# Kernel optimization log

Hardware: AMD Instinct MI355X
Metric: run time of the kernel (lower is better)

Reference implementation:

```python
import jax, jax.numpy as jnp
import numpy as np

BS, NQ, D, NH, NP, L, DFF = 4, 1024, 256, 8, 4, 6, 1024
H_BEV, W_BEV = 200, 150
NV = H_BEV * W_BEV
DH = D // NH


def setup_inputs() -> dict:
    key = jax.random.key(0)
    ks = iter(jax.random.split(key, 64))
    r = lambda *s: jax.random.normal(next(ks), s, dtype=jnp.float32)
    return {
        'query': r(BS, NQ, D),
        'query_pos': r(BS, NQ, D),
        'reference_points': jax.random.uniform(next(ks), (BS, NQ, 1, 2), dtype=jnp.float32),
        'src': r(BS, NV, D),
        'spatial_shapes': jnp.array([[H_BEV, W_BEV]], dtype=jnp.int32),
        'level_start_index': jnp.array([0], dtype=jnp.int32),
        'sa_in_w': r(L, 3 * D, D) * 0.02, 'sa_in_b': jnp.zeros((L, 3 * D), jnp.float32),
        'sa_out_w': r(L, D, D) * 0.02, 'sa_out_b': jnp.zeros((L, D), jnp.float32),
        'ca_off_w': r(L, NH * NP * 2, D) * 0.01, 'ca_off_b': r(L, NH * NP * 2) * 0.5,
        'ca_aw_w': r(L, NH * NP, D) * 0.01, 'ca_aw_b': jnp.zeros((L, NH * NP), jnp.float32),
        'ca_val_w': r(L, D, D) * 0.02, 'ca_val_b': jnp.zeros((L, D), jnp.float32),
        'ca_out_w': r(L, D, D) * 0.02, 'ca_out_b': jnp.zeros((L, D), jnp.float32),
        'n1_w': jnp.ones((L, D), jnp.float32), 'n1_b': jnp.zeros((L, D), jnp.float32),
        'n2_w': jnp.ones((L, D), jnp.float32), 'n2_b': jnp.zeros((L, D), jnp.float32),
        'n3_w': jnp.ones((L, D), jnp.float32), 'n3_b': jnp.zeros((L, D), jnp.float32),
        'ff1_w': r(L, DFF, D) * 0.02, 'ff1_b': jnp.zeros((L, DFF), jnp.float32),
        'ff2_w': r(L, D, DFF) * 0.02, 'ff2_b': jnp.zeros((L, D), jnp.float32),
    }


def layer_norm(x, w, b, eps=1e-5):
    m = jnp.mean(x, -1, keepdims=True)
    v = jnp.mean(jnp.square(x - m), -1, keepdims=True)
    return (x - m) / jnp.sqrt(v + eps) * w + b


def mha_self(x_qk, x_v, in_w, in_b, out_w, out_b):
    bs, nq, d = x_qk.shape
    qw, kw, vw = jnp.split(in_w, 3, axis=0)
    qb, kb, vb = jnp.split(in_b, 3, axis=0)
    q = (x_qk @ qw.T + qb).reshape(bs, nq, NH, DH)
    k = (x_qk @ kw.T + kb).reshape(bs, nq, NH, DH)
    v = (x_v @ vw.T + vb).reshape(bs, nq, NH, DH)
    att = jax.nn.softmax(jnp.einsum('bqhd,bkhd->bhqk', q, k) / jnp.sqrt(jnp.float32(DH)), axis=-1)
    o = jnp.einsum('bhqk,bkhd->bqhd', att, v).reshape(bs, nq, d)
    return o @ out_w.T + out_b


def msda(q, ref, src, lsi0, off_w, off_b, aw_w, aw_b, val_w, val_b, out_w, out_b):
    # single-level (n_levels=1) multi-scale deformable attention, grid_sample
    # bilinear with align_corners=False and zero padding, as in mmcv.
    bs, nq, d = q.shape
    v = (src @ val_w.T + val_b).reshape(bs, NV, NH, DH)
    vt = v.transpose(0, 2, 1, 3)  # (bs, NH, NV, DH)
    off = (q @ off_w.T + off_b).reshape(bs, nq, NH, NP, 2)
    aw = jax.nn.softmax((q @ aw_w.T + aw_b).reshape(bs, nq, NH, NP), axis=-1)
    norm = jnp.array([W_BEV, H_BEV], dtype=q.dtype)  # offset_normalizer = (W, H)
    loc = ref[:, :, None, 0, None, :] + off / norm  # (bs, nq, NH, NP, 2) in [0,1]
    x = loc[..., 0] * W_BEV - 0.5
    y = loc[..., 1] * H_BEV - 0.5
    x0 = jnp.floor(x)
    y0 = jnp.floor(y)
    acc = jnp.zeros((bs, NH, nq, NP, DH), q.dtype)
    for dx, dy in ((0, 0), (1, 0), (0, 1), (1, 1)):
        xi = x0 + dx
        yi = y0 + dy
        w = (1.0 - jnp.abs(x - xi)) * (1.0 - jnp.abs(y - yi))
        valid = (xi >= 0) & (xi < W_BEV) & (yi >= 0) & (yi < H_BEV)
        w = jnp.where(valid, w, 0.0)  # (bs, nq, NH, NP)
        xi_c = jnp.clip(xi, 0, W_BEV - 1).astype(jnp.int32)
        yi_c = jnp.clip(yi, 0, H_BEV - 1).astype(jnp.int32)
        idx = lsi0 + yi_c * W_BEV + xi_c  # flat index into NV
        idx_t = idx.transpose(0, 2, 1, 3).reshape(bs, NH, nq * NP)
        g = jnp.take_along_axis(vt, idx_t[..., None], axis=2).reshape(bs, NH, nq, NP, DH)
        acc = acc + g * w.transpose(0, 2, 1, 3)[..., None]
    o = jnp.einsum('bhqpd,bqhp->bqhd', acc, aw).reshape(bs, nq, d)
    return o @ out_w.T + out_b


def _forward(query, query_pos, reference_points, src,
             sa_in_w, sa_in_b, sa_out_w, sa_out_b,
             ca_off_w, ca_off_b, ca_aw_w, ca_aw_b, ca_val_w, ca_val_b, ca_out_w, ca_out_b,
             n1_w, n1_b, n2_w, n2_b, n3_w, n3_b,
             ff1_w, ff1_b, ff2_w, ff2_b,
             spatial_shapes, level_start_index):
    lsi0 = level_start_index[0]
    out = query
    inter = []
    for l in range(L):
        qk = out + query_pos
        sa = mha_self(qk, out, sa_in_w[l], sa_in_b[l], sa_out_w[l], sa_out_b[l])
        out = layer_norm(out + sa, n2_w[l], n2_b[l])
        ca = msda(out + query_pos, reference_points, src, lsi0,
                  ca_off_w[l], ca_off_b[l], ca_aw_w[l], ca_aw_b[l],
                  ca_val_w[l], ca_val_b[l], ca_out_w[l], ca_out_b[l])
        out = layer_norm(out + ca, n1_w[l], n1_b[l])
        ff = jax.nn.relu(out @ ff1_w[l].T + ff1_b[l]) @ ff2_w[l].T + ff2_b[l]
        out = layer_norm(out + ff, n3_w[l], n3_b[l])
        inter.append(out)
    hs = jnp.stack(inter)  # (L, bs, nq, D)
    refs = jnp.stack([reference_points] * L)  # (L, bs, nq, 1, 2)
    return hs, refs


def reference(query, query_pos, reference_points, src, spatial_shapes, level_start_index,
              sa_in_w, sa_in_b, sa_out_w, sa_out_b,
              ca_off_w, ca_off_b, ca_aw_w, ca_aw_b, ca_val_w, ca_val_b, ca_out_w, ca_out_b,
              n1_w, n1_b, n2_w, n2_b, n3_w, n3_b,
              ff1_w, ff1_b, ff2_w, ff2_b):
    return _forward(query, query_pos, reference_points, src,
                    sa_in_w, sa_in_b, sa_out_w, sa_out_b,
                    ca_off_w, ca_off_b, ca_aw_w, ca_aw_b, ca_val_w, ca_val_b, ca_out_w, ca_out_b,
                    n1_w, n1_b, n2_w, n2_b, n3_w, n3_b,
                    ff1_w, ff1_b, ff2_w, ff2_b,
                    spatial_shapes, level_start_index)
```

## Files before the change

### kernel.cpp

```cpp
#include <hip/hip_runtime.h>

typedef __attribute__((ext_vector_type(8))) short short8;
typedef __attribute__((ext_vector_type(4))) float f32x4;
typedef unsigned short u16;

#define DEVI static __device__ __forceinline__

DEVI float b2f(u16 u){ unsigned int x = ((unsigned int)u) << 16; float f; __builtin_memcpy(&f, &x, 4); return f; }
DEVI u16 f2b(float f){ unsigned int u; __builtin_memcpy(&u, &f, 4); u += 0x7fffu + ((u >> 16) & 1u); return (u16)(u >> 16); }
DEVI short8 cvt8(const float* __restrict__ p){
  f32x4 a = *(const f32x4*)p;
  f32x4 b = *(const f32x4*)(p + 4);
  short8 r;
  r[0]=(short)f2b(a[0]); r[1]=(short)f2b(a[1]); r[2]=(short)f2b(a[2]); r[3]=(short)f2b(a[3]);
  r[4]=(short)f2b(b[0]); r[5]=(short)f2b(b[1]); r[6]=(short)f2b(b[2]); r[7]=(short)f2b(b[3]);
  return r;
}

__global__ __launch_bounds__(256) void cvtall_k(
    const float* __restrict__ sa_in_w, const float* __restrict__ sa_out_w,
    const float* __restrict__ val_w,   const float* __restrict__ cout_w,
    const float* __restrict__ ff1w,    const float* __restrict__ ff2w,
    const float* __restrict__ off_w,   const float* __restrict__ aw_w,
    const float* __restrict__ off_b,   const float* __restrict__ aw_b,
    const float* __restrict__ src,
    u16* __restrict__ wsa_b, u16* __restrict__ wsao_b, u16* __restrict__ wval_b,
    u16* __restrict__ wcao_b, u16* __restrict__ wff1_b, u16* __restrict__ wff2_b,
    u16* __restrict__ wofaw, float* __restrict__ obc, u16* __restrict__ src_b)
{
  long u = (long)blockIdx.x * 256 + threadIdx.x;
  if (u < 147456) { ((short8*)wsa_b)[u]  = cvt8(sa_in_w  + u * 8); return; } u -= 147456;
  if (u < 49152)  { ((short8*)wsao_b)[u] = cvt8(sa_out_w + u * 8); return; } u -= 49152;
  if (u < 49152)  { ((short8*)wval_b)[u] = cvt8(val_w    + u * 8); return; } u -= 49152;
  if (u < 49152)  { ((short8*)wcao_b)[u] = cvt8(cout_w   + u * 8); return; } u -= 49152;
  if (u < 196608) { ((short8*)wff1_b)[u] = cvt8(ff1w     + u * 8); return; } u -= 196608;
  if (u < 196608) { ((short8*)wff2_b)[u] = cvt8(ff2w     + u * 8); return; } u -= 196608;
  if (u < 12288)  { long e = u * 8; int l = (int)(e >> 14); long rem = e & 16383;
                    ((short8*)wofaw)[(l * 24576 + rem) >> 3] = cvt8(off_w + e); return; } u -= 12288;
  if (u < 6144)   { long e = u * 8; int l = (int)(e >> 13); long rem = e & 8191;
                    ((short8*)wofaw)[(l * 24576 + 16384 + rem) >> 3] = cvt8(aw_w + e); return; } u -= 6144;
  if (u < 3840000){ ((short8*)src_b)[u]  = cvt8(src + u * 8); return; } u -= 3840000;
  if (u < 72) {
    long e0 = u * 8;
#pragma unroll
    for (int j = 0; j < 8; j++) {
      long e = e0 + j;
      if (e < 384) { int l = (int)(e >> 6); obc[l * 96 + (e & 63)] = off_b[e]; }
      else { long e2 = e - 384; int l = (int)(e2 >> 5); obc[l * 96 + 64 + (e2 & 31)] = aw_b[e2]; }
    }
  }
}

template<int MT, bool RELU, bool OUTBF, bool VT, bool LN>
__global__ __launch_bounds__(256) void gemm_w_k(
    const u16* __restrict__ A, int lda,
    const u16* __restrict__ W, long wZ,
    const float* __restrict__ bias, int bZ,
    void* __restrict__ Cv, int ldo, long cZ,
    int K,
    u16* __restrict__ vt,
    const float* __restrict__ res,
    const float* __restrict__ lnw, const float* __restrict__ lnb,
    const float* __restrict__ qpos,
    float* __restrict__ out_f, u16* __restrict__ out_b16,
    u16* __restrict__ qk_b16, float* __restrict__ hsp)
{
  __shared__ u16 As[32 * MT * 8];
  __shared__ float r1s[4][64], r2s[4][64], mArr[64], iArr[64];
  const int wave = threadIdx.x >> 6, lane = threadIdx.x & 63;
  const int bm = blockIdx.x * MT;
  const int bn = blockIdx.y * 256 + wave * 64;
  const int lr = lane & 15, lq = lane >> 4;
  constexpr int SH = (MT == 64) ? 6 : 5;
  const u16* Wz = W + (long)blockIdx.z * wZ;
  const float* bz = bias + (long)blockIdx.z * bZ;
  f32x4 acc[MT / 16][4] = {};
  const int nchunks = K >> 8;
  for (int ch = 0; ch < nchunks; ch++) {
#pragma unroll
    for (int it = 0; it < MT / 8; it++) {
      int ub = wave * (MT * 8) + it * 64;
      int u = ub + lane;
      int row = u & (MT - 1), kgrp = u >> SH;
      const u16* ga = A + (long)(bm + row) * lda + ch * 256 + kgrp * 8;
      __builtin_amdgcn_global_load_lds(
          (const __attribute__((address_space(1))) void*)ga,
          (__attribute__((address_space(3))) void*)(As + ub * 8), 16, 0, 0);
    }
    __syncthreads();
#pragma unroll
    for (int s = 0; s < 8; s++) {
      short8 af[MT / 16], bf[4];
#pragma unroll
      for (int i = 0; i < MT / 16; i++)
        af[i] = *(const short8*)(As + ((s * 4 + lq) * MT + i * 16 + lr) * 8);
#pragma unroll
      for (int j = 0; j < 4; j++) {
        int cc = bn + j * 16 + lr;
        bf[j] = *(const short8*)(Wz + (long)cc * K + ch * 256 + s * 32 + lq * 8);
      }
#pragma unroll
      for (int i = 0; i < MT / 16; i++)
#pragma unroll
        for (int j = 0; j < 4; j++)
          acc[i][j] = __builtin_amdgcn_mfma_f32_16x16x32_bf16(af[i], bf[j], acc[i][j], 0, 0, 0);
    }
    __syncthreads();
  }

  float bv[4];
#pragma unroll
  for (int j = 0; j < 4; j++) bv[j] = bz[bn + j * 16 + lr];

  if (!LN) {
    char* Cz = (char*)Cv;
#pragma unroll
    for (int j = 0; j < 4; j++) {
      int cc = bn + j * 16 + lr;
#pragma unroll
      for (int i = 0; i < MT / 16; i++) {
#pragma unroll
        for (int r = 0; r < 4; r++) {
          int rr = bm + i * 16 + lq * 4 + r;
          float v = acc[i][j][r] + bv[j];
          if (RELU) v = fmaxf(v, 0.f);
          long idx = (long)blockIdx.z * cZ + (long)rr * ldo + cc;
          if (OUTBF) ((u16*)Cz)[idx] = f2b(v);
          else       ((float*)Cz)[idx] = v;
          if (VT) {
            int b_ = rr >> 10, q_ = rr & 1023, h_ = cc >> 5, dh_ = cc & 31;
            vt[(long)((((b_ << 3) + h_) << 5) + dh_) * 1024 + q_] = f2b(v);
          }
        }
      }
    }
  } else {
    float s1[MT / 16][4] = {}, s2[MT / 16][4] = {};
#pragma unroll
    for (int i = 0; i < MT / 16; i++) {
#pragma unroll
      for (int r = 0; r < 4; r++) {
        int rowg = bm + i * 16 + lq * 4 + r;
#pragma unroll
        for (int j = 0; j < 4; j++) {
          int cc = bn + j * 16 + lr;
          float x = acc[i][j][r] + bv[j] + res[(long)rowg * 256 + cc];
          s1[i][r] += x; s2[i][r] += x * x;
        }
      }
    }
#pragma unroll
    for (int i = 0; i < MT / 16; i++)
#pragma unroll
      for (int r = 0; r < 4; r++) {
#pragma unroll
        for (int m = 1; m <= 8; m <<= 1) {
          s1[i][r] += __shfl_xor(s1[i][r], m);
          s2[i][r] += __shfl_xor(s2[i][r], m);
        }
      }
    if (lr == 0) {
#pragma unroll
      for (int i = 0; i < MT / 16; i++)
#pragma unroll
        for (int r = 0; r < 4; r++) {
          int rl = i * 16 + lq * 4 + r;
          r1s[wave][rl] = s1[i][r];
          r2s[wave][rl] = s2[i][r];
        }
    }
    __syncthreads();
    if (threadIdx.x < MT) {
      int t = threadIdx.x;
      float a = r1s[0][t] + r1s[1][t] + r1s[2][t] + r1s[3][t];
      float b = r2s[0][t] + r2s[1][t] + r2s[2][t] + r2s[3][t];
      float m = a * (1.f / 256.f);
      float var = b * (1.f / 256.f) - m * m;
      mArr[t] = m;
      iArr[t] = rsqrtf(var + 1e-5f);
    }
    __syncthreads();
#pragma unroll
    for (int i = 0; i < MT / 16; i++) {
#pragma unroll
      for (int r = 0; r < 4; r++) {
        int rl = i * 16 + lq * 4 + r;
        int rowg = bm + rl;
        float m = mArr[rl], inv = iArr[rl];
#pragma unroll
        for (int j = 0; j < 4; j++) {
          int cc = bn + j * 16 + lr;
          long idx = (long)rowg * 256 + cc;
          float x = acc[i][j][r] + bv[j] + res[idx];
          float y = (x - m) * inv * lnw[cc] + lnb[cc];
          out_f[idx] = y;
          if (out_b16) out_b16[idx] = f2b(y);
          if (qk_b16)  qk_b16[idx]  = f2b(y + qpos[idx]);
          if (hsp)     hsp[idx]     = y;
        }
      }
    }
  }
}

__global__ __launch_bounds__(256) void qkv_k(
    const u16* __restrict__ qk_b, const u16* __restrict__ out_b,
    const u16* __restrict__ wsa, const float* __restrict__ bsa,
    u16* __restrict__ qkbuf, u16* __restrict__ vt)
{
  __shared__ u16 As[32 * 64 * 8];
  const int sel = blockIdx.y;
  const u16* A = (sel == 2) ? out_b : qk_b;
  const u16* W = wsa + (long)sel * 256 * 256;
  const int wave = threadIdx.x >> 6, lane = threadIdx.x & 63;
  const int bm = blockIdx.x * 64;
  const int bn = wave * 64;
  const int lr = lane & 15, lq = lane >> 4;
  f32x4 acc[4][4] = {};
#pragma unroll
  for (int it = 0; it < 8; it++) {
    int ub = wave * 512 + it * 64;
    int u = ub + lane;
    int row = u & 63, kgrp = u >> 6;
    const u16* ga = A + (long)(bm + row) * 256 + kgrp * 8;
    __builtin_amdgcn_global_load_lds(
        (const __attribute__((address_space(1))) void*)ga,
        (__attribute__((address_space(3))) void*)(As + ub * 8), 16, 0, 0);
  }
  __syncthreads();
#pragma unroll
  for (int s = 0; s < 8; s++) {
    short8 af[4], bf[4];
#pragma unroll
    for (int i = 0; i < 4; i++)
      af[i] = *(const short8*)(As + ((s * 4 + lq) * 64 + i * 16 + lr) * 8);
#pragma unroll
    for (int j = 0; j < 4; j++) {
      int cc = bn + j * 16 + lr;
      bf[j] = *(const short8*)(W + (long)cc * 256 + s * 32 + lq * 8);
    }
#pragma unroll
    for (int i = 0; i < 4; i++)
#pragma unroll
      for (int j = 0; j < 4; j++)
        acc[i][j] = __builtin_amdgcn_mfma_f32_16x16x32_bf16(af[i], bf[j], acc[i][j], 0, 0, 0);
  }
  float bv[4];
#pragma unroll
  for (int j = 0; j < 4; j++) bv[j] = bsa[sel * 256 + bn + j * 16 + lr];
#pragma unroll
  for (int j = 0; j < 4; j++) {
    int cc = bn + j * 16 + lr;
#pragma unroll
    for (int i = 0; i < 4; i++) {
#pragma unroll
      for (int r = 0; r < 4; r++) {
        int rr = bm + i * 16 + lq * 4 + r;
        float v = acc[i][j][r] + bv[j];
        if (sel < 2) {
          qkbuf[(long)rr * 512 + sel * 256 + cc] = f2b(v);
        } else {
          int b_ = rr >> 10, q_ = rr & 1023, h_ = cc >> 5, dh_ = cc & 31;
          vt[(long)((((b_ << 3) + h_) << 5) + dh_) * 1024 + q_] = f2b(v);
        }
      }
    }
  }
}

__global__ __launch_bounds__(256) void flash_k(
    const u16* __restrict__ qkbuf, const u16* __restrict__ vt,
    u16* __restrict__ obuf)
{
  const float SC = 0.17677669529663687f;
  __shared__ u16 Plds[4][32][136];
  const int bh = blockIdx.x >> 3;
  const int b = bh >> 3, h = bh & 7;
  const int qt = blockIdx.x & 7;
  const int wave = threadIdx.x >> 6, lane = threadIdx.x & 63;
  const int lr = lane & 15, lq = lane >> 4;
  const int qbase = qt * 128 + wave * 32;

  short8 qf[2];
#pragma unroll
  for (int i = 0; i < 2; i++)
    qf[i] = *(const short8*)(qkbuf + (long)(b * 1024 + qbase + i * 16 + lr) * 512 + h * 32 + lq * 8);

  const u16* Kb = qkbuf + (long)b * 1024 * 512 + 256 + h * 32;
  const u16* Vb = vt + (long)bh * 32 * 1024;

  f32x4 acc_o[2][2] = {};
  float m_run[2][4], l_run[2][4];
#pragma unroll
  for (int i = 0; i < 2; i++)
#pragma unroll
    for (int r = 0; r < 4; r++){ m_run[i][r] = -3e38f; l_run[i][r] = 0.f; }

  for (int kt = 0; kt < 8; kt++) {
    f32x4 s[2][8] = {};
#pragma unroll
    for (int j = 0; j < 8; j++) {
      short8 kf = *(const short8*)(Kb + (long)(kt * 128 + j * 16 + lr) * 512 + lq * 8);
#pragma unroll
      for (int i = 0; i < 2; i++)
        s[i][j] = __builtin_amdgcn_mfma_f32_16x16x32_bf16(qf[i], kf, s[i][j], 0, 0, 0);
    }
#pragma unroll
    for (int i = 0; i < 2; i++) {
#pragma unroll
      for (int r = 0; r < 4; r++) {
        float mx = s[i][0][r];
#pragma unroll
        for (int j = 1; j < 8; j++) mx = fmaxf(mx, s[i][j][r]);
#pragma unroll
        for (int m = 1; m <= 8; m <<= 1) mx = fmaxf(mx, __shfl_xor(mx, m));
        float m_new = fmaxf(m_run[i][r], mx);
        float alpha = __expf((m_run[i][r] - m_new) * SC);
        float sum = 0.f;
        int row = i * 16 + lq * 4 + r;
#pragma unroll
        for (int j = 0; j < 8; j++) {
          float p = __expf((s[i][j][r] - m_new) * SC);
          sum += p;
          Plds[wave][row][j * 16 + lr] = f2b(p);
        }
#pragma unroll
        for (int m = 1; m <= 8; m <<= 1) sum += __shfl_xor(sum, m);
        l_run[i][r] = l_run[i][r] * alpha + sum;
        m_run[i][r] = m_new;
#pragma unroll
        for (int d = 0; d < 2; d++) acc_o[i][d][r] *= alpha;
      }
    }
#pragma unroll
    for (int kc = 0; kc < 4; kc++) {
      short8 pf[2];
#pragma unroll
      for (int i = 0; i < 2; i++)
        pf[i] = *(const short8*)&Plds[wave][i * 16 + lr][kc * 32 + lq * 8];
#pragma unroll
      for (int d = 0; d < 2; d++) {
        short8 vf = *(const short8*)(Vb + (long)(d * 16 + lr) * 1024 + kt * 128 + kc * 32 + lq * 8);
#pragma unroll
        for (int i = 0; i < 2; i++)
          acc_o[i][d] = __builtin_amdgcn_mfma_f32_16x16x32_bf16(pf[i], vf, acc_o[i][d], 0, 0, 0);
      }
    }
  }
#pragma unroll
  for (int i = 0; i < 2; i++) {
#pragma unroll
    for (int r = 0; r < 4; r++) {
      float inv = 1.f / l_run[i][r];
      int q = qbase + i * 16 + lq * 4 + r;
#pragma unroll
      for (int d = 0; d < 2; d++)
        obuf[(long)(b * 1024 + q) * 256 + h * 32 + d * 16 + lr] = f2b(acc_o[i][d][r] * inv);
    }
  }
}

__global__ __launch_bounds__(256) void gemm64_k(
    const u16* __restrict__ A, int lda,
    const u16* __restrict__ W, int ldw,
    const float* __restrict__ bias,
    float* __restrict__ C, int ldo,
    int M, int N, int K)
{
  const int wave = threadIdx.x >> 6, lane = threadIdx.x & 63;
  const int wm = wave >> 1, wn = wave & 1;
  const int bm = blockIdx.x * 64 + wm * 32;
  const int bn = blockIdx.y * 64 + wn * 32;
  const int lr = lane & 15, lq = lane >> 4;
  const int koff = lq * 8;
  f32x4 acc[2][2] = {};
  const short8 Z8 = {0,0,0,0,0,0,0,0};
  for (int k0 = 0; k0 < K; k0 += 32) {
    short8 af[2], bf[2];
#pragma unroll
    for (int i = 0; i < 2; i++) {
      int r = bm + i * 16 + lr;
      af[i] = (r < M) ? *(const short8*)(A + (long)r * lda + k0 + koff) : Z8;
    }
#pragma unroll
    for (int j = 0; j < 2; j++) {
      int c = bn + j * 16 + lr;
      bf[j] = (c < N) ? *(const short8*)(W + (long)c * ldw + k0 + koff) : Z8;
    }
#pragma unroll
    for (int i = 0; i < 2; i++)
#pragma unroll
      for (int j = 0; j < 2; j++)
        acc[i][j] = __builtin_amdgcn_mfma_f32_16x16x32_bf16(af[i], bf[j], acc[i][j], 0, 0, 0);
  }
#pragma unroll
  for (int j = 0; j < 2; j++) {
    int cc = bn + j * 16 + lr;
    if (cc >= N) continue;
    float bv = bias[cc];
#pragma unroll
    for (int i = 0; i < 2; i++) {
#pragma unroll
      for (int r = 0; r < 4; r++) {
        int rr = bm + i * 16 + lq * 4 + r;
        if (rr >= M) continue;
        C[(long)rr * ldo + cc] = acc[i][j][r] + bv;
      }
    }
  }
}

__global__ __launch_bounds__(256) void init_prep_k(const float* __restrict__ q, const float* __restrict__ qpos,
                                                   float* __restrict__ out_f, u16* __restrict__ out_b,
                                                   u16* __restrict__ qk_b){
  long i = (long)blockIdx.x * 256 + threadIdx.x;
  float o = q[i];
  out_f[i] = o;
  out_b[i] = f2b(o);
  qk_b[i]  = f2b(o + qpos[i]);
}

__global__ __launch_bounds__(256) void msda_k(
    const float* __restrict__ refp,
    const float* __restrict__ off, int ldoff,
    const float* __restrict__ aw, int ldaw,
    const u16* __restrict__ v,
    u16* __restrict__ o,
    long vstride)
{
  int tid = blockIdx.x * 256 + threadIdx.x;
  int dh = tid & 31;
  int h  = (tid >> 5) & 7;
  int bq = tid >> 8;
  int b  = bq >> 10;
  float rx = refp[bq * 2 + 0];
  float ry = refp[bq * 2 + 1];
  const float* offp = off + (long)bq * ldoff + h * 8;
  const float* awp  = aw  + (long)bq * ldaw + h * 4;
  float a0 = awp[0], a1 = awp[1], a2 = awp[2], a3 = awp[3];
  float am = fmaxf(fmaxf(a0, a1), fmaxf(a2, a3));
  float e[4];
  e[0] = __expf(a0 - am); e[1] = __expf(a1 - am); e[2] = __expf(a2 - am); e[3] = __expf(a3 - am);
  float einv = 1.f / (e[0] + e[1] + e[2] + e[3]);
  const u16* vb = v + b * vstride + h * 32 + dh;
  float accv = 0.f;
#pragma unroll
  for (int pp = 0; pp < 4; pp++){
    float x = rx * 150.f + offp[pp * 2 + 0] - 0.5f;
    float y = ry * 200.f + offp[pp * 2 + 1] - 0.5f;
    float x0 = floorf(x), y0 = floorf(y);
    float s = 0.f;
#pragma unroll
    for (int c = 0; c < 4; c++){
      int dx = c & 1, dy = c >> 1;
      float xi = x0 + dx, yi = y0 + dy;
      float wt = (1.f - fabsf(x - xi)) * (1.f - fabsf(y - yi));
      if (xi >= 0.f && xi < 150.f && yi >= 0.f && yi < 200.f && wt > 0.f) {
        int xc = (int)xi, yc = (int)yi;
        s += wt * b2f(vb[((long)yc * 150 + xc) * 256]);
      }
    }
    accv += e[pp] * einv * s;
  }
  o[(long)bq * 256 + h * 32 + dh] = f2b(accv);
}

__global__ __launch_bounds__(256) void refs_k(const float* __restrict__ r, float* __restrict__ dst){
  int i = blockIdx.x * 256 + threadIdx.x;
  dst[i] = r[i & 8191];
}

extern "C" void kernel_launch(void* const* d_in, const int* in_sizes, int n_in,
                              void* d_out, int out_size, void* d_ws, size_t ws_size,
                              hipStream_t stream)
{
  (void)in_sizes; (void)n_in; (void)out_size;
  const float* query = (const float*)d_in[0];
  const float* qpos  = (const float*)d_in[1];
  const float* refp  = (const float*)d_in[2];
  const float* src   = (const float*)d_in[3];
  const float* sa_in_w  = (const float*)d_in[6];
  const float* sa_in_b  = (const float*)d_in[7];
  const float* sa_out_w = (const float*)d_in[8];
  const float* sa_out_b = (const float*)d_in[9];
  const float* off_w = (const float*)d_in[10];
  const float* off_b = (const float*)d_in[11];
  const float* aw_w  = (const float*)d_in[12];
  const float* aw_b  = (const float*)d_in[13];
  const float* val_w = (const float*)d_in[14];
  const float* val_b = (const float*)d_in[15];
  const float* cout_w = (const float*)d_in[16];
  const float* cout_b = (const float*)d_in[17];
  const float* n1w = (const float*)d_in[18]; const float* n1b = (const float*)d_in[19];
  const float* n2w = (const float*)d_in[20]; const float* n2b = (const float*)d_in[21];
  const float* n3w = (const float*)d_in[22]; const float* n3b = (const float*)d_in[23];
  const float* ff1w = (const float*)d_in[24]; const float* ff1b = (const float*)d_in[25];
  const float* ff2w = (const float*)d_in[26]; const float* ff2b = (const float*)d_in[27];

  float* hs = (float*)d_out;
  float* refs_out = hs + (long)6 * 4096 * 256;

  char* p = (char*)d_ws;
  auto alloc = [&](size_t bytes){ char* r = p; p += (bytes + 255) & ~(size_t)255; return r; };
  float* out_f = (float*)alloc(4194304);
  u16*   qk_b  = (u16*)  alloc(2097152);
  u16*   out_b = (u16*)  alloc(2097152);
  u16* wsa_b  = (u16*)alloc(2359296);
  u16* wsao_b = (u16*)alloc(786432);
  u16* wofaw  = (u16*)alloc(294912);
  u16* wval_b = (u16*)alloc(786432);
  u16* wcao_b = (u16*)alloc(786432);
  u16* wff1_b = (u16*)alloc(3145728);
  u16* wff2_b = (u16*)alloc(3145728);
  float* obc  = (float*)alloc(2304);
  u16* src_b  = (u16*)alloc(61440000);
  u16* qkbuf  = (u16*)alloc(4194304);
  u16* vt     = (u16*)alloc(2097152);
  u16* obuf   = (u16*)alloc(2097152);
  float* oawo = (float*)alloc(1572864);
  u16* mo     = (u16*)alloc(2097152);
  u16* ffh    = (u16*)alloc(8388608);
  size_t used = (size_t)(p - (char*)d_ws);
  const bool big = (ws_size >= used + 368640000ull);
  u16* vsrc = (u16*)alloc(big ? 368640000ull : 61440000ull);

  init_prep_k<<<4096, 256, 0, stream>>>(query, qpos, out_f, out_b, qk_b);
  cvtall_k<<<17761, 256, 0, stream>>>(sa_in_w, sa_out_w, val_w, cout_w, ff1w, ff2w,
                                      off_w, aw_w, off_b, aw_b, src,
                                      wsa_b, wsao_b, wval_b, wcao_b, wff1_b, wff2_b,
                                      wofaw, obc, src_b);
  if (big) {
    gemm_w_k<64,false,true,false,false><<<dim3(1875,1,6),256,0,stream>>>(
        src_b, 256, wval_b, 65536, val_b, 256, vsrc, 256, 30720000, 256,
        nullptr, nullptr,nullptr,nullptr,nullptr,nullptr,nullptr,nullptr,nullptr);
  }

  for (int l = 0; l < 6; l++){
    const u16* wsa = wsa_b + (long)l * 768 * 256;
    qkv_k<<<dim3(64,3,1),256,0,stream>>>(qk_b, out_b, wsa, sa_in_b + l * 768, qkbuf, vt);
    flash_k<<<256,256,0,stream>>>(qkbuf, vt, obuf);
    gemm_w_k<32,false,false,false,true><<<dim3(128,1,1),256,0,stream>>>(
        obuf, 256, wsao_b + (long)l*65536, 0, sa_out_b + l*256, 0, nullptr, 0, 0, 256,
        nullptr, out_f, n2w + l*256, n2b + l*256, qpos, out_f, nullptr, qk_b, nullptr);
    gemm64_k<<<dim3(64,2,1),256,0,stream>>>(qk_b, 256, wofaw + (long)l*24576, 256,
        obc + l*96, oawo, 96, 4096, 96, 256);
    if (!big) {
      gemm_w_k<64,false,true,false,false><<<dim3(1875,1,1),256,0,stream>>>(
          src_b, 256, wval_b + (long)l*65536, 0, val_b + l*256, 0, vsrc, 256, 0, 256,
          nullptr, nullptr,nullptr,nullptr,nullptr,nullptr,nullptr,nullptr,nullptr);
    }
    const u16* vsl = big ? (vsrc + (long)l*30720000) : vsrc;
    msda_k<<<4096,256,0,stream>>>(refp, oawo, 96, oawo + 64, 96, vsl, mo, 7680000);
    gemm_w_k<32,false,false,false,true><<<dim3(128,1,1),256,0,stream>>>(
        mo, 256, wcao_b + (long)l*65536, 0, cout_b + l*256, 0, nullptr, 0, 0, 256,
        nullptr, out_f, n1w + l*256, n1b + l*256, nullptr, out_f, out_b, nullptr, nullptr);
    gemm_w_k<64,true,true,false,false><<<dim3(64,4,1),256,0,stream>>>(
        out_b, 256, wff1_b + (long)l*262144, 0, ff1b + l*1024, 0, ffh, 1024, 0, 256,
        nullptr, nullptr,nullptr,nullptr,nullptr,nullptr,nullptr,nullptr,nullptr);
    gemm_w_k<32,false,false,false,true><<<dim3(128,1,1),256,0,stream>>>(
        ffh, 1024, wff2_b + (long)l*262144, 0, ff2b + l*256, 0, nullptr, 0, 0, 1024,
        nullptr, out_f, n3w + l*256, n3b + l*256, qpos, out_f, out_b, qk_b,
        hs + (long)l*1048576);
  }
  refs_k<<<192,256,0,stream>>>(refp, refs_out);
}
```

Baseline: 1.707 ms.

## Fuse six-layer value projection into one A-tile-reusing kernel and merge init prep

```diff
diff --git a/kernel.cpp b/kernel.cpp
--- a/kernel.cpp
+++ b/kernel.cpp
@@ -24,9 +24,11 @@
     const float* __restrict__ off_w,   const float* __restrict__ aw_w,
     const float* __restrict__ off_b,   const float* __restrict__ aw_b,
     const float* __restrict__ src,
+    const float* __restrict__ query,   const float* __restrict__ qpos,
     u16* __restrict__ wsa_b, u16* __restrict__ wsao_b, u16* __restrict__ wval_b,
     u16* __restrict__ wcao_b, u16* __restrict__ wff1_b, u16* __restrict__ wff2_b,
-    u16* __restrict__ wofaw, float* __restrict__ obc, u16* __restrict__ src_b)
+    u16* __restrict__ wofaw, float* __restrict__ obc, u16* __restrict__ src_b,
+    float* __restrict__ out_f, u16* __restrict__ out_b, u16* __restrict__ qk_b)
 {
   long u = (long)blockIdx.x * 256 + threadIdx.x;
   if (u < 147456) { ((short8*)wsa_b)[u]  = cvt8(sa_in_w  + u * 8); return; } u -= 147456;
@@ -48,6 +50,76 @@
       if (e < 384) { int l = (int)(e >> 6); obc[l * 96 + (e & 63)] = off_b[e]; }
       else { long e2 = e - 384; int l = (int)(e2 >> 5); obc[l * 96 + 64 + (e2 & 31)] = aw_b[e2]; }
     }
+    return;
+  } u -= 72;
+  if (u < 131072) {
+    long e = u * 8;
+#pragma unroll
+    for (int j = 0; j < 8; j++) {
+      float o = query[e + j];
+      out_f[e + j] = o;
+      out_b[e + j] = f2b(o);
+      qk_b[e + j]  = f2b(o + qpos[e + j]);
+    }
+  }
+}
+
+__global__ __launch_bounds__(256) void val6_k(
+    const u16* __restrict__ A,
+    const u16* __restrict__ W,
+    const float* __restrict__ bias,
+    u16* __restrict__ C)
+{
+  __shared__ u16 As[32 * 64 * 8];
+  const int wave = threadIdx.x >> 6, lane = threadIdx.x & 63;
+  const int bm = blockIdx.x * 64;
+  const int bn = wave * 64;
+  const int lr = lane & 15, lq = lane >> 4;
+#pragma unroll
+  for (int it = 0; it < 8; it++) {
+    int ub = wave * 512 + it * 64;
+    int u = ub + lane;
+    int row = u & 63, kgrp = u >> 6;
+    const u16* ga = A + (long)(bm + row) * 256 + kgrp * 8;
+    __builtin_amdgcn_global_load_lds(
+        (const __attribute__((address_space(1))) void*)ga,
+        (__attribute__((address_space(3))) void*)(As + ub * 8), 16, 0, 0);
+  }
+  __syncthreads();
+  for (int l = 0; l < 6; l++) {
+    const u16* Wl = W + (long)l * 65536;
+    f32x4 acc[4][4] = {};
+#pragma unroll
+    for (int s = 0; s < 8; s++) {
+      short8 af[4], bf[4];
+#pragma unroll
+      for (int i = 0; i < 4; i++)
+        af[i] = *(const short8*)(As + ((s * 4 + lq) * 64 + i * 16 + lr) * 8);
+#pragma unroll
+      for (int j = 0; j < 4; j++) {
+        int cc = bn + j * 16 + lr;
+        bf[j] = *(const short8*)(Wl + (long)cc * 256 + s * 32 + lq * 8);
+      }
+#pragma unroll
+      for (int i = 0; i < 4; i++)
+#pragma unroll
+        for (int j = 0; j < 4; j++)
+          acc[i][j] = __builtin_amdgcn_mfma_f32_16x16x32_bf16(af[i], bf[j], acc[i][j], 0, 0, 0);
+    }
+    u16* Cl = C + (long)l * 30720000;
+    const float* bl = bias + l * 256;
+#pragma unroll
+    for (int j = 0; j < 4; j++) {
+      int cc = bn + j * 16 + lr;
+      float bv = bl[cc];
+#pragma unroll
+      for (int i = 0; i < 4; i++)
+#pragma unroll
+        for (int r = 0; r < 4; r++) {
+          int rr = bm + i * 16 + lq * 4 + r;
+          Cl[(long)rr * 256 + cc] = f2b(acc[i][j][r] + bv);
+        }
+    }
   }
 }
 
@@ -408,16 +480,6 @@
       }
     }
   }
-}
-
-__global__ __launch_bounds__(256) void init_prep_k(const float* __restrict__ q, const float* __restrict__ qpos,
-                                                   float* __restrict__ out_f, u16* __restrict__ out_b,
-                                                   u16* __restrict__ qk_b){
-  long i = (long)blockIdx.x * 256 + threadIdx.x;
-  float o = q[i];
-  out_f[i] = o;
-  out_b[i] = f2b(o);
-  qk_b[i]  = f2b(o + qpos[i]);
 }
 
 __global__ __launch_bounds__(256) void msda_k(
@@ -524,15 +586,12 @@
   const bool big = (ws_size >= used + 368640000ull);
   u16* vsrc = (u16*)alloc(big ? 368640000ull : 61440000ull);
 
-  init_prep_k<<<4096, 256, 0, stream>>>(query, qpos, out_f, out_b, qk_b);
-  cvtall_k<<<17761, 256, 0, stream>>>(sa_in_w, sa_out_w, val_w, cout_w, ff1w, ff2w,
-                                      off_w, aw_w, off_b, aw_b, src,
+  cvtall_k<<<18273, 256, 0, stream>>>(sa_in_w, sa_out_w, val_w, cout_w, ff1w, ff2w,
+                                      off_w, aw_w, off_b, aw_b, src, query, qpos,
                                       wsa_b, wsao_b, wval_b, wcao_b, wff1_b, wff2_b,
-                                      wofaw, obc, src_b);
+                                      wofaw, obc, src_b, out_f, out_b, qk_b);
   if (big) {
-    gemm_w_k<64,false,true,false,false><<<dim3(1875,1,6),256,0,stream>>>(
-        src_b, 256, wval_b, 65536, val_b, 256, vsrc, 256, 30720000, 256,
-        nullptr, nullptr,nullptr,nullptr,nullptr,nullptr,nullptr,nullptr,nullptr);
+    val6_k<<<1875, 256, 0, stream>>>(src_b, wval_b, val_b, vsrc);
   }
 
   for (int l = 0; l < 6; l++){
@@ -554,7 +613,7 @@
     gemm_w_k<32,false,false,false,true><<<dim3(128,1,1),256,0,stream>>>(
         mo, 256, wcao_b + (long)l*65536, 0, cout_b + l*256, 0, nullptr, 0, 0, 256,
         nullptr, out_f, n1w + l*256, n1b + l*256, nullptr, out_f, out_b, nullptr, nullptr);
-    gemm_w_k<64,true,true,false,false><<<dim3(64,4,1),256,0,stream>>>(
+    gemm_w_k<32,true,true,false,false><<<dim3(128,4,1),256,0,stream>>>(
         out_b, 256, wff1_b + (long)l*262144, 0, ff1b + l*1024, 0, ffh, 1024, 0, 256,
         nullptr, nullptr,nullptr,nullptr,nullptr,nullptr,nullptr,nullptr,nullptr);
     gemm_w_k<32,false,false,false,true><<<dim3(128,1,1),256,0,stream>>>(
```

After: 1.745 ms. 2.2% more time.
